# Optimization experiments

Hardware: AMD Instinct MI355X
Metric: run time of the kernel (lower is better)

The kernel has to match this reference:

```python
import jax, jax.numpy as jnp
import numpy as np

B, N, F_IN, H = 16, 1024, 64, 256
NEG = -9e15
ALPHA = 0.2  # LeakyReLU slope


def _leaky(x):
    return jnp.where(x >= 0, x, ALPHA * x)


def setup_inputs() -> dict:
    key = jax.random.key(0)
    ks = jax.random.split(key, 12)
    s = lambda k, shape, fan: jax.random.normal(k, shape, jnp.float32) / np.sqrt(fan)
    node_features = jax.random.normal(ks[0], (B, N, F_IN), jnp.float32)
    adj_matrix = jax.random.randint(ks[1], (B, N, N), 0, 2).astype(jnp.float32)
    return {
        "node_features": node_features,
        "adj_matrix": adj_matrix,
        "emb_W": s(ks[2], (F_IN, H), F_IN),
        "emb_b": jnp.zeros((H,), jnp.float32),
        "W0": s(ks[3], (H, H), H),
        "a1_0": s(ks[4], (H,), H),
        "a2_0": s(ks[5], (H,), H),
        "W1": s(ks[6], (H, H), H),
        "a1_1": s(ks[7], (H,), H),
        "a2_1": s(ks[8], (H,), H),
        "gp_W1": s(ks[9], (H, H), H),
        "gp_b1": jnp.zeros((H,), jnp.float32),
        "gp_W2": s(ks[10], (H, H), H),
        "gp_b2": jnp.zeros((H,), jnp.float32),
    }


def _gat_layer(x, mask, W, a1, a2):
    # x: [B,N,H]; mask: [B,N,N] bool. Equivalent to original concat trick:
    # a([h_i || h_j]) = h_i @ a1 + h_j @ a2 with a.weight split in halves.
    h = jnp.einsum('bnf,fo->bno', x, W)              # [B,N,H]
    s1 = jnp.einsum('bnh,h->bn', h, a1)              # [B,N]
    s2 = jnp.einsum('bnh,h->bn', h, a2)              # [B,N]
    e = _leaky(s1[:, :, None] + s2[:, None, :])      # [B,N,N]
    att = jax.nn.softmax(jnp.where(mask, e, NEG), axis=2)
    # dropout p=0.2 is identity in eval mode
    return jnp.einsum('bij,bjh->bih', att, h)        # [B,N,H]


def reference(node_features, adj_matrix, emb_W, emb_b,
              W0, a1_0, a2_0, W1, a1_1, a2_1,
              gp_W1, gp_b1, gp_W2, gp_b2):
    mask = adj_matrix > 0
    x = jnp.einsum('bnf,fh->bnh', node_features, emb_W) + emb_b
    x = jax.nn.relu(_gat_layer(x, mask, W0, a1_0, a2_0))
    x = jax.nn.relu(_gat_layer(x, mask, W1, a1_1, a2_1))
    g = jnp.mean(x, axis=1) + jnp.max(x, axis=1)     # [B,H]
    g = jax.nn.relu(g @ gp_W1 + gp_b1) @ gp_W2 + gp_b2
    return x, g
```

## Files before the change

kernel.cpp:

```cpp
#include <hip/hip_runtime.h>
#include <hip/hip_bf16.h>

#define B 16
#define N 1024
#define F_IN 64
#define H 256
#define ALPHA 0.2f

typedef __attribute__((ext_vector_type(8))) short short8;
typedef __attribute__((ext_vector_type(8))) _Float16 half8;
typedef __attribute__((ext_vector_type(4))) _Float16 half4;
typedef __attribute__((ext_vector_type(4))) float floatx4;

__device__ __forceinline__ floatx4 mfma_f16(half8 a, half8 b, floatx4 c) {
    return __builtin_amdgcn_mfma_f32_16x16x32_f16(a, b, c, 0, 0, 0);
}

__global__ __launch_bounds__(256) void k_front(const float* __restrict__ adj,
                                               const float* __restrict__ nf,
                                               const float* __restrict__ embW,
                                               const float* __restrict__ embB,
                                               const float* __restrict__ W0, const float* __restrict__ W1,
                                               const float* __restrict__ a10, const float* __restrict__ a20,
                                               const float* __restrict__ a11, const float* __restrict__ a21,
                                               unsigned* __restrict__ mask32,
                                               _Float16* __restrict__ xf,
                                               _Float16* __restrict__ wBf,
                                               float* __restrict__ wa1, float* __restrict__ wa2) {
    __shared__ float lds[256 * 17];
    const int blk = blockIdx.x;
    const int t = threadIdx.x;
    const int lane = t & 63;

    if (blk < 1024) {
        const int wv = blk * 4 + (t >> 6);
#pragma unroll 2
        for (int task = wv; task < B * N * 4; task += 4096) {
            const float4 v = *(const float4*)(adj + (size_t)task * 256 + lane * 4);
            unsigned long long b0 = __ballot(v.x > 0.f);
            unsigned long long b1 = __ballot(v.y > 0.f);
            unsigned long long b2 = __ballot(v.z > 0.f);
            unsigned long long b3 = __ballot(v.w > 0.f);
            if (lane < 8) {
                unsigned w0 = (unsigned)((b0 >> (8 * lane)) & 0xff)
                            | ((unsigned)((b1 >> (8 * lane)) & 0xff) << 8)
                            | ((unsigned)((b2 >> (8 * lane)) & 0xff) << 16)
                            | ((unsigned)((b3 >> (8 * lane)) & 0xff) << 24);
                const int jg = task & 3, row = task >> 2;
                mask32[(size_t)row * 32 + jg * 8 + lane] = w0;
            }
        }
        return;
    }
    if (blk < 1536) {
        const int row0 = (blk - 1024) * 32;
        float* nfs = lds;
        for (int idx = t; idx < 32 * F_IN; idx += 256) {
            int r = idx >> 6, f = idx & 63;
            nfs[f * 32 + r] = nf[(size_t)(row0 + r) * F_IN + f];
        }
        __syncthreads();
        const int c = t;
        float acc[32];
        const float bv = embB[c];
#pragma unroll
        for (int r = 0; r < 32; r++) acc[r] = bv;
#pragma unroll 8
        for (int f = 0; f < F_IN; f++) {
            const float w = embW[f * H + c];
            const float* nrow = nfs + f * 32;
#pragma unroll
            for (int q = 0; q < 8; q++) {
                float4 n4 = *(const float4*)(nrow + q * 4);
                acc[q * 4 + 0] += n4.x * w;
                acc[q * 4 + 1] += n4.y * w;
                acc[q * 4 + 2] += n4.z * w;
                acc[q * 4 + 3] += n4.w * w;
            }
        }
#pragma unroll
        for (int r = 0; r < 32; r++)
            xf[(size_t)(row0 + r) * H + c] = (_Float16)acc[r];
        return;
    }
    const int pb = blk - 1536;
    if (pb >= 32) {
        const int l = pb - 32;
        const float* W = l ? W1 : W0;
        const float* a1 = l ? a11 : a10;
        const float* a2 = l ? a21 : a20;
        float* a1s = lds;
        float* a2s = lds + 256;
        a1s[t] = a1[t]; a2s[t] = a2[t];
        __syncthreads();
        float v1 = 0.f, v2 = 0.f;
        for (int c = 0; c < H; c += 4) {
            float4 w = *(const float4*)&W[t * H + c];
            v1 += w.x * a1s[c] + w.y * a1s[c + 1] + w.z * a1s[c + 2] + w.w * a1s[c + 3];
            v2 += w.x * a2s[c] + w.y * a2s[c + 1] + w.z * a2s[c + 2] + w.w * a2s[c + 3];
        }
        wa1[l * H + t] = v1;
        wa2[l * H + t] = v2;
        return;
    }
    const int l = pb >> 4, ct = pb & 15;
    const float* W = l ? W1 : W0;
#pragma unroll
    for (int rep = 0; rep < 16; rep++) {
        int idx = rep * 256 + t;
        int k = idx >> 4, cl = idx & 15;
        lds[k * 17 + cl] = W[k * H + ct * 16 + cl];
    }
    __syncthreads();
    const int w = t >> 6;
    const int l15 = lane & 15, quad = lane >> 4;
#pragma unroll
    for (int e = 0; e < 2; e++) {
        const int ks = w * 2 + e;
        half8 bf;
#pragma unroll
        for (int jj = 0; jj < 8; jj++)
            bf[jj] = (_Float16)lds[(ks * 32 + quad * 8 + jj) * 17 + l15];
        *(half8*)(wBf + (size_t)(((l * 16 + ct) * 8 + ks) * 64 + lane) * 8) = bf;
    }
}

#define XS(it, ks) ((((it) * 8 + (ks))) * 520)
__global__ __launch_bounds__(256, 4) void k_gemm(const _Float16* __restrict__ xf,
                                                 const _Float16* __restrict__ wBf,
                                                 const float* __restrict__ wa1, const float* __restrict__ wa2,
                                                 _Float16* __restrict__ hB,
                                                 float* __restrict__ s1, float* __restrict__ s2,
                                                 unsigned* __restrict__ s2maxkey) {
    __shared__ __align__(16) _Float16 sm[8320];
    const int lin = blockIdx.x;
    const int rc = lin >> 1, chalf = lin & 1;
    const int row0 = rc * 32;
    const int t = threadIdx.x;
    const int lane = t & 63, w = t >> 6;
    const int l15 = lane & 15, quad = lane >> 4;

#pragma unroll
    for (int pass = 0; pass < 4; pass++) {
        int idx = pass * 256 + t;
        int row_l = idx >> 5, k8 = idx & 31;
        half8 v = *(const half8*)(xf + (size_t)(row0 + row_l) * H + k8 * 8);
        int it = row_l >> 4, lf = row_l & 15, ks = k8 >> 2, qd = k8 & 3;
        *(half8*)(sm + XS(it, ks) + (qd * 16 + lf) * 8) = v;
    }
    __syncthreads();

    const int ct0 = chalf * 8 + 2 * w;
    const _Float16* pB0 = wBf + (size_t)((ct0 * 8) * 64 + lane) * 8;
    const _Float16* pB1 = wBf + (size_t)(((ct0 + 1) * 8) * 64 + lane) * 8;

    floatx4 acc[2][2];
    floatx4 z = {0.f, 0.f, 0.f, 0.f};
    acc[0][0] = z; acc[0][1] = z; acc[1][0] = z; acc[1][1] = z;
    float sp1a = 0.f, sp2a = 0.f, sp1b = 0.f, sp2b = 0.f;

    half8 B0 = *(const half8*)(pB0);
    half8 B1 = *(const half8*)(pB1);

#pragma unroll
    for (int ks = 0; ks < 8; ks++) {
        half8 nB0 = B0, nB1 = B1;
        if (ks < 7) {
            const int o = (ks + 1) * 512;
            nB0 = *(const half8*)(pB0 + o);
            nB1 = *(const half8*)(pB1 + o);
        }
        half8 A0 = *(const half8*)(sm + XS(0, ks) + lane * 8);
        half8 A1 = *(const half8*)(sm + XS(1, ks) + lane * 8);
        acc[0][0] = mfma_f16(A0, B0, acc[0][0]);
        acc[0][1] = mfma_f16(A0, B1, acc[0][1]);
        acc[1][0] = mfma_f16(A1, B0, acc[1][0]);
        acc[1][1] = mfma_f16(A1, B1, acc[1][1]);
        if (chalf == 0 && w == 0) {
            float4 w1a = *(const float4*)(wa1 + ks * 32 + quad * 8);
            float4 w1b = *(const float4*)(wa1 + ks * 32 + quad * 8 + 4);
            float4 w2a = *(const float4*)(wa2 + ks * 32 + quad * 8);
            float4 w2b = *(const float4*)(wa2 + ks * 32 + quad * 8 + 4);
            float wv1[8] = {w1a.x, w1a.y, w1a.z, w1a.w, w1b.x, w1b.y, w1b.z, w1b.w};
            float wv2[8] = {w2a.x, w2a.y, w2a.z, w2a.w, w2b.x, w2b.y, w2b.z, w2b.w};
#pragma unroll
            for (int j = 0; j < 8; j++) {
                float xa = (float)A0[j];
                float xb = (float)A1[j];
                sp1a += xa * wv1[j]; sp2a += xa * wv2[j];
                sp1b += xb * wv1[j]; sp2b += xb * wv2[j];
            }
        }
        B0 = nB0; B1 = nB1;
    }

    __syncthreads();
    _Float16* trc = sm;
#pragma unroll
    for (int rg = 0; rg < 2; rg++) {
#pragma unroll
        for (int n2 = 0; n2 < 2; n2++) {
            const int c_l = (2 * w + n2) * 16 + l15;
            half4 hv;
            hv[0] = (_Float16)acc[rg][n2][0];
            hv[1] = (_Float16)acc[rg][n2][1];
            hv[2] = (_Float16)acc[rg][n2][2];
            hv[3] = (_Float16)acc[rg][n2][3];
            *(half4*)(trc + c_l * 40 + rg * 16 + quad * 4) = hv;
        }
    }
    __syncthreads();
    {
        const int ct_l = t >> 5, sub = t & 31;
        const int bb = row0 >> 10, jt = (row0 >> 5) & 31;
        _Float16* dst = hB + (size_t)(((bb * 16 + chalf * 8 + ct_l) * 32 + jt) * 64) * 8;
#pragma unroll
        for (int rep = 0; rep < 2; rep++) {
            int lo = sub + rep * 32;
            int qd = lo >> 4, lf = lo & 15;
            half8 hv = *(const half8*)(trc + (ct_l * 16 + lf) * 40 + qd * 8);
            *(half8*)(dst + lo * 8) = hv;
        }
    }
    if (chalf == 0 && w == 0) {
        sp1a += __shfl_xor(sp1a, 16); sp1a += __shfl_xor(sp1a, 32);
        sp2a += __shfl_xor(sp2a, 16); sp2a += __shfl_xor(sp2a, 32);
        sp1b += __shfl_xor(sp1b, 16); sp1b += __shfl_xor(sp1b, 32);
        sp2b += __shfl_xor(sp2b, 16); sp2b += __shfl_xor(sp2b, 32);
        if (quad == 0) {
            s1[row0 + l15] = sp1a; s2[row0 + l15] = sp2a;
            s1[row0 + 16 + l15] = sp1b; s2[row0 + 16 + l15] = sp2b;
        }
        float m = fmaxf(sp2a, sp2b);
#pragma unroll
        for (int off = 1; off <= 8; off <<= 1) m = fmaxf(m, __shfl_xor(m, off));
        if (lane == 0) {
            unsigned bt = __float_as_uint(m);
            unsigned keyv = (bt & 0x80000000u) ? ~bt : (bt | 0x80000000u);
            atomicMax(&s2maxkey[row0 >> 10], keyv);
        }
    }
}

__global__ __launch_bounds__(256) void k_pgen(const float* __restrict__ s1, const float* __restrict__ s2,
                                              const unsigned* __restrict__ mask32,
                                              const unsigned* __restrict__ s2maxkey,
                                              _Float16* __restrict__ pA, float* __restrict__ lsums) {
    __shared__ float s2s[N];
    __shared__ float lp[4][16];
    const int lin = blockIdx.x;
    const int xcd = lin & 7, sl = lin >> 3;
    const int b = xcd * 2 + (sl & 1);
    const int itg = sl >> 1;
    const int t = threadIdx.x;
    const int lane = t & 63, w = t >> 6;
    const int l15 = lane & 15, quad = lane >> 4;

    unsigned key = s2maxkey[b];
    unsigned mb = (key & 0x80000000u) ? (key ^ 0x80000000u) : ~key;
    const float s2max = __uint_as_float(mb);
    for (int idx = t; idx < N; idx += 256) s2s[idx] = s2[b * N + idx];
    __syncthreads();

    const int it = itg * 2 + (w & 1);
    const int jt0 = (w >> 1) * 16;
    const int i = it * 16 + l15;
    const float s1v = s1[b * N + i];
    const float tmx = s1v + s2max;
    const float mrow = fmaxf(tmx, ALPHA * tmx);
    const unsigned* mp = mask32 + (size_t)(b * N + i) * 32;
    _Float16* pdst = pA + (size_t)(((b * 64 + it) * 32 + jt0) * 64) * 8 + lane * 8;
    const int qsh = quad * 2;
    float lacc = 0.f;

    for (int jl = 0; jl < 16; jl++) {
        const int jt = jt0 + jl;
        unsigned mw = mp[jt];
        float4 sa = *(const float4*)&s2s[jt * 32 + quad * 8];
        float4 sb = *(const float4*)&s2s[jt * 32 + quad * 8 + 4];
        float sv[8] = {sa.x, sa.y, sa.z, sa.w, sb.x, sb.y, sb.z, sb.w};
        union { _Float16 h[8]; half8 v; } pk;
#pragma unroll
        for (int jj = 0; jj < 8; jj++) {
            float e = s1v + sv[jj];
            e = fmaxf(e, ALPHA * e);
            float p = __expf(e - mrow);
            p = ((mw >> ((jj & 3) * 8 + (jj >> 2) + qsh)) & 1u) ? p : 0.f;
            pk.h[jj] = (_Float16)p;
            lacc += (float)pk.h[jj];
        }
        *(half8*)(pdst + (size_t)jl * 512) = pk.v;
    }
    lacc += __shfl_xor(lacc, 16);
    lacc += __shfl_xor(lacc, 32);
    if (quad == 0) lp[w][l15] = lacc;
    __syncthreads();
    if (t < 32) {
        int itl = t >> 4, lf = t & 15;
        float tot = lp[itl][lf] + lp[2 + itl][lf];
        lsums[b * N + (itg * 2 + itl) * 16 + lf] = tot;
    }
}

template <int LAST>
__global__ __launch_bounds__(256, 2) void k_gat(const _Float16* __restrict__ pA,
                                                const _Float16* __restrict__ hB,
                                                const float* __restrict__ lsums,
                                                float* __restrict__ outf,
                                                _Float16* __restrict__ oxf,
                                                float* __restrict__ psum, float* __restrict__ pmax) {
    const int lin = blockIdx.x;
    const int xcd = lin & 7, sl = lin >> 3;
    const int b = xcd * 2 + (sl & 1);
    const int chunk = (sl >> 1) & 15;
    const int chalf = sl >> 5;
    const int i0 = chunk * 64;
    const int t = threadIdx.x;
    const int lane = t & 63, w = t >> 6;
    const int l15 = lane & 15, quad = lane >> 4;
    const int nb = 2 * w;
    const int ct0 = chalf * 8 + nb;

    const _Float16* pa0 = pA + (size_t)((b * 64 + chunk * 4 + 0) * 32 * 64) * 8 + lane * 8;
    const _Float16* pa1 = pA + (size_t)((b * 64 + chunk * 4 + 1) * 32 * 64) * 8 + lane * 8;
    const _Float16* pa2 = pA + (size_t)((b * 64 + chunk * 4 + 2) * 32 * 64) * 8 + lane * 8;
    const _Float16* pa3 = pA + (size_t)((b * 64 + chunk * 4 + 3) * 32 * 64) * 8 + lane * 8;
    const _Float16* pb0 = hB + (size_t)((b * 16 + ct0) * 32 * 64) * 8 + lane * 8;
    const _Float16* pb1 = hB + (size_t)((b * 16 + ct0 + 1) * 32 * 64) * 8 + lane * 8;

    floatx4 acc[4][2];
    floatx4 z = {0.f, 0.f, 0.f, 0.f};
#pragma unroll
    for (int rg = 0; rg < 4; rg++) { acc[rg][0] = z; acc[rg][1] = z; }

    half8 cA0 = *(const half8*)(pa0), cA1 = *(const half8*)(pa1);
    half8 cA2 = *(const half8*)(pa2), cA3 = *(const half8*)(pa3);
    half8 cB0 = *(const half8*)(pb0), cB1 = *(const half8*)(pb1);
    half8 nA0 = *(const half8*)(pa0 + 512), nA1 = *(const half8*)(pa1 + 512);
    half8 nA2 = *(const half8*)(pa2 + 512), nA3 = *(const half8*)(pa3 + 512);
    half8 nB0 = *(const half8*)(pb0 + 512), nB1 = *(const half8*)(pb1 + 512);

#pragma unroll 2
    for (int jt = 0; jt < 32; jt++) {
        const int j2 = (jt + 2 <= 31 ? jt + 2 : 31) * 512;
        half8 fA0 = *(const half8*)(pa0 + j2);
        half8 fA1 = *(const half8*)(pa1 + j2);
        half8 fA2 = *(const half8*)(pa2 + j2);
        half8 fA3 = *(const half8*)(pa3 + j2);
        half8 fB0 = *(const half8*)(pb0 + j2);
        half8 fB1 = *(const half8*)(pb1 + j2);
        acc[0][0] = mfma_f16(cA0, cB0, acc[0][0]);
        acc[1][0] = mfma_f16(cA1, cB0, acc[1][0]);
        acc[2][0] = mfma_f16(cA2, cB0, acc[2][0]);
        acc[3][0] = mfma_f16(cA3, cB0, acc[3][0]);
        acc[0][1] = mfma_f16(cA0, cB1, acc[0][1]);
        acc[1][1] = mfma_f16(cA1, cB1, acc[1][1]);
        acc[2][1] = mfma_f16(cA2, cB1, acc[2][1]);
        acc[3][1] = mfma_f16(cA3, cB1, acc[3][1]);
        cA0 = nA0; cA1 = nA1; cA2 = nA2; cA3 = nA3; cB0 = nB0; cB1 = nB1;
        nA0 = fA0; nA1 = fA1; nA2 = fA2; nA3 = fA3; nB0 = fB0; nB1 = fB1;
    }

    const size_t rbase = (size_t)b * N + i0;
    float inv[4][4];
#pragma unroll
    for (int rg = 0; rg < 4; rg++)
#pragma unroll
        for (int r = 0; r < 4; r++) inv[rg][r] = 1.f / lsums[rbase + rg * 16 + quad * 4 + r];

    float colsum[2] = {0.f, 0.f}, colmax[2] = {-INFINITY, -INFINITY};
#pragma unroll
    for (int rg = 0; rg < 4; rg++)
#pragma unroll
        for (int n2 = 0; n2 < 2; n2++) {
            const int c = (ct0 + n2) * 16 + l15;
#pragma unroll
            for (int r = 0; r < 4; r++) {
                float v = fmaxf(acc[rg][n2][r] * inv[rg][r], 0.f);
                const size_t row = rbase + rg * 16 + quad * 4 + r;
                if (LAST) {
                    outf[row * H + c] = v;
                    colsum[n2] += v;
                    colmax[n2] = fmaxf(colmax[n2], v);
                } else {
                    oxf[row * H + c] = (_Float16)v;
                }
            }
        }
    if (LAST) {
#pragma unroll
        for (int n2 = 0; n2 < 2; n2++) {
            float s = colsum[n2], m = colmax[n2];
            s += __shfl_xor(s, 16); s += __shfl_xor(s, 32);
            m = fmaxf(m, __shfl_xor(m, 16)); m = fmaxf(m, __shfl_xor(m, 32));
            if (quad == 0) {
                const int c = (ct0 + n2) * 16 + l15;
                psum[(b * 16 + chunk) * H + c] = s;
                pmax[(b * 16 + chunk) * H + c] = m;
            }
        }
    }
}

__global__ __launch_bounds__(256) void k_pool2(const float* __restrict__ psum,
                                               const float* __restrict__ pmax,
                                               const float* __restrict__ W1, const float* __restrict__ b1,
                                               const float* __restrict__ W2, const float* __restrict__ b2,
                                               float* __restrict__ gout) {
    __shared__ float g_s[H];
    __shared__ float t_s[H];
    const int b = blockIdx.x;
    const int c = threadIdx.x;
    float s = 0.f, m = -INFINITY;
#pragma unroll
    for (int ch = 0; ch < 16; ch++) {
        s += psum[(b * 16 + ch) * H + c];
        m = fmaxf(m, pmax[(b * 16 + ch) * H + c]);
    }
    g_s[c] = s * (1.f / N) + m;
    __syncthreads();
    float a = b1[c];
#pragma unroll 16
    for (int k = 0; k < H; k++) a += g_s[k] * W1[k * H + c];
    t_s[c] = fmaxf(a, 0.f);
    __syncthreads();
    float o = b2[c];
#pragma unroll 16
    for (int k = 0; k < H; k++) o += t_s[k] * W2[k * H + c];
    gout[b * H + c] = o;
}

extern "C" void kernel_launch(void* const* d_in, const int* in_sizes, int n_in,
                              void* d_out, int out_size, void* d_ws, size_t ws_size,
                              hipStream_t stream) {
    const float* nf    = (const float*)d_in[0];
    const float* adj   = (const float*)d_in[1];
    const float* emb_W = (const float*)d_in[2];
    const float* emb_b = (const float*)d_in[3];
    const float* W0    = (const float*)d_in[4];
    const float* a1_0  = (const float*)d_in[5];
    const float* a2_0  = (const float*)d_in[6];
    const float* W1    = (const float*)d_in[7];
    const float* a1_1  = (const float*)d_in[8];
    const float* a2_1  = (const float*)d_in[9];
    const float* gpW1  = (const float*)d_in[10];
    const float* gpb1  = (const float*)d_in[11];
    const float* gpW2  = (const float*)d_in[12];
    const float* gpb2  = (const float*)d_in[13];

    float* xout = (float*)d_out;
    float* gout = xout + B * N * H;

    char* w = (char*)d_ws;
    _Float16* xf     = (_Float16*)(w);
    _Float16* hB     = (_Float16*)(w + 8388608);
    _Float16* pA     = (_Float16*)(w + 16777216);
    unsigned* mask32 = (unsigned*)(w + 50331648);
    float* s1        = (float*)(w + 52428800);
    float* s2        = (float*)(w + 52494336);
    float* lsums     = (float*)(w + 52559872);
    _Float16* wBf    = (_Float16*)(w + 52625408);
    float* wa1       = (float*)(w + 52887552);
    float* wa2       = (float*)(w + 52889600);
    unsigned* keys   = (unsigned*)(w + 52891648);
    float* psum      = (float*)(w);
    float* pmax      = (float*)(w + 262144);

    hipMemsetAsync(keys, 0, 128, stream);
    k_front<<<1570, 256, 0, stream>>>(adj, nf, emb_W, emb_b, W0, W1,
                                      a1_0, a2_0, a1_1, a2_1,
                                      mask32, xf, wBf, wa1, wa2);

    k_gemm<<<1024, 256, 0, stream>>>(xf, wBf, wa1, wa2, hB, s1, s2, keys);
    k_pgen<<<512, 256, 0, stream>>>(s1, s2, mask32, keys, pA, lsums);
    k_gat<0><<<512, 256, 0, stream>>>(pA, hB, lsums, nullptr, xf, nullptr, nullptr);

    k_gemm<<<1024, 256, 0, stream>>>(xf, wBf + 65536, wa1 + H, wa2 + H, hB, s1, s2, keys + 16);
    k_pgen<<<512, 256, 0, stream>>>(s1, s2, mask32, keys + 16, pA, lsums);
    k_gat<1><<<512, 256, 0, stream>>>(pA, hB, lsums, xout, nullptr, psum, pmax);

    k_pool2<<<B, 256, 0, stream>>>(psum, pmax, gpW1, gpb1, gpW2, gpb2, gout);
}
```

Before: 243.8 us.

## Fuse attention probability generation and pooling head into the GAT aggregation kernel

Removes the separate probability-generation kernel and its large fp16 attention matrix in global memory. Each GAT block now computes exp-scores from s1/s2 and the bit mask on the fly, builds the MFMA A operand in registers, and accumulates row sums locally. The s2 max moves from a global atomic key to a per-block reduction. The final pooling MLP runs in the last block per batch via an atomic counter, replacing the pool2 launch. In exchange, each block recomputes the exponentials redundantly across its two column halves and holds eight B fragments per wave, which raises register pressure.

After: 275.8 us. +13.1%, slower.

```diff
diff --git a/kernel.cpp b/kernel.cpp
--- a/kernel.cpp
+++ b/kernel.cpp
@@ -7,7 +7,6 @@
 #define H 256
 #define ALPHA 0.2f
 
-typedef __attribute__((ext_vector_type(8))) short short8;
 typedef __attribute__((ext_vector_type(8))) _Float16 half8;
 typedef __attribute__((ext_vector_type(4))) _Float16 half4;
 typedef __attribute__((ext_vector_type(4))) float floatx4;
@@ -130,8 +129,7 @@
                                                  const _Float16* __restrict__ wBf,
                                                  const float* __restrict__ wa1, const float* __restrict__ wa2,
                                                  _Float16* __restrict__ hB,
-                                                 float* __restrict__ s1, float* __restrict__ s2,
-                                                 unsigned* __restrict__ s2maxkey) {
+                                                 float* __restrict__ s1, float* __restrict__ s2) {
     __shared__ __align__(16) _Float16 sm[8320];
     const int lin = blockIdx.x;
     const int rc = lin >> 1, chalf = lin & 1;
@@ -231,84 +229,28 @@
             s1[row0 + l15] = sp1a; s2[row0 + l15] = sp2a;
             s1[row0 + 16 + l15] = sp1b; s2[row0 + 16 + l15] = sp2b;
         }
-        float m = fmaxf(sp2a, sp2b);
-#pragma unroll
-        for (int off = 1; off <= 8; off <<= 1) m = fmaxf(m, __shfl_xor(m, off));
-        if (lane == 0) {
-            unsigned bt = __float_as_uint(m);
-            unsigned keyv = (bt & 0x80000000u) ? ~bt : (bt | 0x80000000u);
-            atomicMax(&s2maxkey[row0 >> 10], keyv);
-        }
     }
 }
 
-__global__ __launch_bounds__(256) void k_pgen(const float* __restrict__ s1, const float* __restrict__ s2,
-                                              const unsigned* __restrict__ mask32,
-                                              const unsigned* __restrict__ s2maxkey,
-                                              _Float16* __restrict__ pA, float* __restrict__ lsums) {
-    __shared__ float s2s[N];
-    __shared__ float lp[4][16];
-    const int lin = blockIdx.x;
-    const int xcd = lin & 7, sl = lin >> 3;
-    const int b = xcd * 2 + (sl & 1);
-    const int itg = sl >> 1;
-    const int t = threadIdx.x;
-    const int lane = t & 63, w = t >> 6;
-    const int l15 = lane & 15, quad = lane >> 4;
-
-    unsigned key = s2maxkey[b];
-    unsigned mb = (key & 0x80000000u) ? (key ^ 0x80000000u) : ~key;
-    const float s2max = __uint_as_float(mb);
-    for (int idx = t; idx < N; idx += 256) s2s[idx] = s2[b * N + idx];
-    __syncthreads();
-
-    const int it = itg * 2 + (w & 1);
-    const int jt0 = (w >> 1) * 16;
-    const int i = it * 16 + l15;
-    const float s1v = s1[b * N + i];
-    const float tmx = s1v + s2max;
-    const float mrow = fmaxf(tmx, ALPHA * tmx);
-    const unsigned* mp = mask32 + (size_t)(b * N + i) * 32;
-    _Float16* pdst = pA + (size_t)(((b * 64 + it) * 32 + jt0) * 64) * 8 + lane * 8;
-    const int qsh = quad * 2;
-    float lacc = 0.f;
-
-    for (int jl = 0; jl < 16; jl++) {
-        const int jt = jt0 + jl;
-        unsigned mw = mp[jt];
-        float4 sa = *(const float4*)&s2s[jt * 32 + quad * 8];
-        float4 sb = *(const float4*)&s2s[jt * 32 + quad * 8 + 4];
-        float sv[8] = {sa.x, sa.y, sa.z, sa.w, sb.x, sb.y, sb.z, sb.w};
-        union { _Float16 h[8]; half8 v; } pk;
-#pragma unroll
-        for (int jj = 0; jj < 8; jj++) {
-            float e = s1v + sv[jj];
-            e = fmaxf(e, ALPHA * e);
-            float p = __expf(e - mrow);
-            p = ((mw >> ((jj & 3) * 8 + (jj >> 2) + qsh)) & 1u) ? p : 0.f;
-            pk.h[jj] = (_Float16)p;
-            lacc += (float)pk.h[jj];
-        }
-        *(half8*)(pdst + (size_t)jl * 512) = pk.v;
-    }
-    lacc += __shfl_xor(lacc, 16);
-    lacc += __shfl_xor(lacc, 32);
-    if (quad == 0) lp[w][l15] = lacc;
-    __syncthreads();
-    if (t < 32) {
-        int itl = t >> 4, lf = t & 15;
-        float tot = lp[itl][lf] + lp[2 + itl][lf];
-        lsums[b * N + (itg * 2 + itl) * 16 + lf] = tot;
-    }
-}
-
 template <int LAST>
-__global__ __launch_bounds__(256, 2) void k_gat(const _Float16* __restrict__ pA,
-                                                const _Float16* __restrict__ hB,
-                                                const float* __restrict__ lsums,
+__global__ __launch_bounds__(256, 2) void k_gat(const _Float16* __restrict__ hB,
+                                                const float* __restrict__ s1g,
+                                                const float* __restrict__ s2g,
+                                                const unsigned* __restrict__ mask32,
                                                 float* __restrict__ outf,
                                                 _Float16* __restrict__ oxf,
-                                                float* __restrict__ psum, float* __restrict__ pmax) {
+                                                float* __restrict__ psum, float* __restrict__ pmax,
+                                                unsigned* __restrict__ cnt,
+                                                const float* __restrict__ gpW1, const float* __restrict__ gpb1,
+                                                const float* __restrict__ gpW2, const float* __restrict__ gpb2,
+                                                float* __restrict__ gout) {
+    __shared__ float s2s[N];
+    __shared__ unsigned msk[64][33];
+    __shared__ float wmax[4];
+    __shared__ float l_s[64];
+    __shared__ float red1[4][128];
+    __shared__ float red2[4][128];
+    __shared__ int flag_s;
     const int lin = blockIdx.x;
     const int xcd = lin & 7, sl = lin >> 3;
     const int b = xcd * 2 + (sl & 1);
@@ -318,116 +260,140 @@
     const int t = threadIdx.x;
     const int lane = t & 63, w = t >> 6;
     const int l15 = lane & 15, quad = lane >> 4;
-    const int nb = 2 * w;
-    const int ct0 = chalf * 8 + nb;
-
-    const _Float16* pa0 = pA + (size_t)((b * 64 + chunk * 4 + 0) * 32 * 64) * 8 + lane * 8;
-    const _Float16* pa1 = pA + (size_t)((b * 64 + chunk * 4 + 1) * 32 * 64) * 8 + lane * 8;
-    const _Float16* pa2 = pA + (size_t)((b * 64 + chunk * 4 + 2) * 32 * 64) * 8 + lane * 8;
-    const _Float16* pa3 = pA + (size_t)((b * 64 + chunk * 4 + 3) * 32 * 64) * 8 + lane * 8;
-    const _Float16* pb0 = hB + (size_t)((b * 16 + ct0) * 32 * 64) * 8 + lane * 8;
-    const _Float16* pb1 = hB + (size_t)((b * 16 + ct0 + 1) * 32 * 64) * 8 + lane * 8;
-
-    floatx4 acc[4][2];
+    const int ct0 = chalf * 8;
+
+    float tm = -INFINITY;
+    for (int idx = t; idx < N; idx += 256) {
+        float v = s2g[b * N + idx];
+        s2s[idx] = v;
+        tm = fmaxf(tm, v);
+    }
+#pragma unroll
+    for (int off = 1; off <= 32; off <<= 1) tm = fmaxf(tm, __shfl_xor(tm, off));
+    if (lane == 0) wmax[w] = tm;
+#pragma unroll
+    for (int pass = 0; pass < 8; pass++) {
+        int idx = pass * 256 + t;
+        int r = idx >> 5, wd = idx & 31;
+        msk[r][wd] = mask32[(size_t)(b * N + i0 + r) * 32 + wd];
+    }
+    __syncthreads();
+    const float s2max = fmaxf(fmaxf(wmax[0], wmax[1]), fmaxf(wmax[2], wmax[3]));
+
+    const float s1v = s1g[b * N + i0 + w * 16 + l15];
+    const float tmx = s1v + s2max;
+    const float mrow = fmaxf(tmx, ALPHA * tmx);
+
+    const _Float16* pb[8];
+#pragma unroll
+    for (int k = 0; k < 8; k++)
+        pb[k] = hB + (size_t)((b * 16 + ct0 + k) * 32 * 64) * 8 + lane * 8;
+
+    floatx4 acc[8];
     floatx4 z = {0.f, 0.f, 0.f, 0.f};
 #pragma unroll
-    for (int rg = 0; rg < 4; rg++) { acc[rg][0] = z; acc[rg][1] = z; }
-
-    half8 cA0 = *(const half8*)(pa0), cA1 = *(const half8*)(pa1);
-    half8 cA2 = *(const half8*)(pa2), cA3 = *(const half8*)(pa3);
-    half8 cB0 = *(const half8*)(pb0), cB1 = *(const half8*)(pb1);
-    half8 nA0 = *(const half8*)(pa0 + 512), nA1 = *(const half8*)(pa1 + 512);
-    half8 nA2 = *(const half8*)(pa2 + 512), nA3 = *(const half8*)(pa3 + 512);
-    half8 nB0 = *(const half8*)(pb0 + 512), nB1 = *(const half8*)(pb1 + 512);
-
-#pragma unroll 2
+    for (int k = 0; k < 8; k++) acc[k] = z;
+    float lacc = 0.f;
+
+    half8 cB[8];
+#pragma unroll
+    for (int k = 0; k < 8; k++) cB[k] = *(const half8*)(pb[k]);
+
     for (int jt = 0; jt < 32; jt++) {
-        const int j2 = (jt + 2 <= 31 ? jt + 2 : 31) * 512;
-        half8 fA0 = *(const half8*)(pa0 + j2);
-        half8 fA1 = *(const half8*)(pa1 + j2);
-        half8 fA2 = *(const half8*)(pa2 + j2);
-        half8 fA3 = *(const half8*)(pa3 + j2);
-        half8 fB0 = *(const half8*)(pb0 + j2);
-        half8 fB1 = *(const half8*)(pb1 + j2);
-        acc[0][0] = mfma_f16(cA0, cB0, acc[0][0]);
-        acc[1][0] = mfma_f16(cA1, cB0, acc[1][0]);
-        acc[2][0] = mfma_f16(cA2, cB0, acc[2][0]);
-        acc[3][0] = mfma_f16(cA3, cB0, acc[3][0]);
-        acc[0][1] = mfma_f16(cA0, cB1, acc[0][1]);
-        acc[1][1] = mfma_f16(cA1, cB1, acc[1][1]);
-        acc[2][1] = mfma_f16(cA2, cB1, acc[2][1]);
-        acc[3][1] = mfma_f16(cA3, cB1, acc[3][1]);
-        cA0 = nA0; cA1 = nA1; cA2 = nA2; cA3 = nA3; cB0 = nB0; cB1 = nB1;
-        nA0 = fA0; nA1 = fA1; nA2 = fA2; nA3 = fA3; nB0 = fB0; nB1 = fB1;
-    }
-
-    const size_t rbase = (size_t)b * N + i0;
-    float inv[4][4];
-#pragma unroll
-    for (int rg = 0; rg < 4; rg++)
-#pragma unroll
-        for (int r = 0; r < 4; r++) inv[rg][r] = 1.f / lsums[rbase + rg * 16 + quad * 4 + r];
-
-    float colsum[2] = {0.f, 0.f}, colmax[2] = {-INFINITY, -INFINITY};
-#pragma unroll
-    for (int rg = 0; rg < 4; rg++)
-#pragma unroll
-        for (int n2 = 0; n2 < 2; n2++) {
-            const int c = (ct0 + n2) * 16 + l15;
-#pragma unroll
-            for (int r = 0; r < 4; r++) {
-                float v = fmaxf(acc[rg][n2][r] * inv[rg][r], 0.f);
-                const size_t row = rbase + rg * 16 + quad * 4 + r;
-                if (LAST) {
-                    outf[row * H + c] = v;
-                    colsum[n2] += v;
-                    colmax[n2] = fmaxf(colmax[n2], v);
-                } else {
-                    oxf[row * H + c] = (_Float16)v;
-                }
+        half8 nB[8];
+        if (jt < 31) {
+            const int o = (jt + 1) * 512;
+#pragma unroll
+            for (int k = 0; k < 8; k++) nB[k] = *(const half8*)(pb[k] + o);
+        }
+        unsigned mwq = msk[w * 16 + l15][jt] >> (quad * 2);
+        float4 sa = *(const float4*)&s2s[jt * 32 + quad * 8];
+        float4 sb = *(const float4*)&s2s[jt * 32 + quad * 8 + 4];
+        float sv[8] = {sa.x, sa.y, sa.z, sa.w, sb.x, sb.y, sb.z, sb.w};
+        union { _Float16 h[8]; half8 v; } pk;
+#pragma unroll
+        for (int jj = 0; jj < 8; jj++) {
+            float e = s1v + sv[jj];
+            e = fmaxf(e, ALPHA * e);
+            float p = __expf(e - mrow);
+            p = ((mwq >> ((jj & 3) * 8 + (jj >> 2))) & 1u) ? p : 0.f;
+            pk.h[jj] = (_Float16)p;
+            lacc += (float)pk.h[jj];
+        }
+        half8 A = pk.v;
+#pragma unroll
+        for (int k = 0; k < 8; k++) acc[k] = mfma_f16(A, cB[k], acc[k]);
+        if (jt < 31) {
+#pragma unroll
+            for (int k = 0; k < 8; k++) cB[k] = nB[k];
+        }
+    }
+
+    lacc += __shfl_xor(lacc, 16);
+    lacc += __shfl_xor(lacc, 32);
+    if (quad == 0) l_s[w * 16 + l15] = lacc;
+    __syncthreads();
+
+    float inv[4];
+#pragma unroll
+    for (int r = 0; r < 4; r++) inv[r] = 1.f / l_s[w * 16 + quad * 4 + r];
+
+    const size_t rbase = (size_t)b * N + i0 + w * 16 + quad * 4;
+#pragma unroll
+    for (int k = 0; k < 8; k++) {
+        const int c = (ct0 + k) * 16 + l15;
+        float cs = 0.f, cm = -INFINITY;
+#pragma unroll
+        for (int r = 0; r < 4; r++) {
+            float v = fmaxf(acc[k][r] * inv[r], 0.f);
+            if (LAST) {
+                outf[(rbase + r) * H + c] = v;
+                cs += v; cm = fmaxf(cm, v);
+            } else {
+                oxf[(rbase + r) * H + c] = (_Float16)v;
             }
         }
+        if (LAST) {
+            cs += __shfl_xor(cs, 16); cs += __shfl_xor(cs, 32);
+            cm = fmaxf(cm, __shfl_xor(cm, 16)); cm = fmaxf(cm, __shfl_xor(cm, 32));
+            if (quad == 0) { red1[w][k * 16 + l15] = cs; red2[w][k * 16 + l15] = cm; }
+        }
+    }
     if (LAST) {
-#pragma unroll
-        for (int n2 = 0; n2 < 2; n2++) {
-            float s = colsum[n2], m = colmax[n2];
-            s += __shfl_xor(s, 16); s += __shfl_xor(s, 32);
-            m = fmaxf(m, __shfl_xor(m, 16)); m = fmaxf(m, __shfl_xor(m, 32));
-            if (quad == 0) {
-                const int c = (ct0 + n2) * 16 + l15;
-                psum[(b * 16 + chunk) * H + c] = s;
-                pmax[(b * 16 + chunk) * H + c] = m;
+        __syncthreads();
+        if (t < 128) {
+            float s = red1[0][t] + red1[1][t] + red1[2][t] + red1[3][t];
+            float m = fmaxf(fmaxf(red2[0][t], red2[1][t]), fmaxf(red2[2][t], red2[3][t]));
+            psum[(b * 16 + chunk) * H + chalf * 128 + t] = s;
+            pmax[(b * 16 + chunk) * H + chalf * 128 + t] = m;
+        }
+        __threadfence();
+        __syncthreads();
+        if (t == 0) flag_s = (int)atomicAdd(&cnt[b], 1u);
+        __syncthreads();
+        if (flag_s == 31) {
+            __threadfence();
+            float* g_s = s2s;
+            float* t_s = s2s + 256;
+            float s = 0.f, m = -INFINITY;
+#pragma unroll
+            for (int ch = 0; ch < 16; ch++) {
+                s += psum[(b * 16 + ch) * H + t];
+                m = fmaxf(m, pmax[(b * 16 + ch) * H + t]);
             }
-        }
-    }
-}
-
-__global__ __launch_bounds__(256) void k_pool2(const float* __restrict__ psum,
-                                               const float* __restrict__ pmax,
-                                               const float* __restrict__ W1, const float* __restrict__ b1,
-                                               const float* __restrict__ W2, const float* __restrict__ b2,
-                                               float* __restrict__ gout) {
-    __shared__ float g_s[H];
-    __shared__ float t_s[H];
-    const int b = blockIdx.x;
-    const int c = threadIdx.x;
-    float s = 0.f, m = -INFINITY;
-#pragma unroll
-    for (int ch = 0; ch < 16; ch++) {
-        s += psum[(b * 16 + ch) * H + c];
-        m = fmaxf(m, pmax[(b * 16 + ch) * H + c]);
-    }
-    g_s[c] = s * (1.f / N) + m;
-    __syncthreads();
-    float a = b1[c];
+            g_s[t] = s * (1.f / N) + m;
+            __syncthreads();
+            float a = gpb1[t];
 #pragma unroll 16
-    for (int k = 0; k < H; k++) a += g_s[k] * W1[k * H + c];
-    t_s[c] = fmaxf(a, 0.f);
-    __syncthreads();
-    float o = b2[c];
+            for (int k = 0; k < H; k++) a += g_s[k] * gpW1[k * H + t];
+            t_s[t] = fmaxf(a, 0.f);
+            __syncthreads();
+            float o = gpb2[t];
 #pragma unroll 16
-    for (int k = 0; k < H; k++) o += t_s[k] * W2[k * H + c];
-    gout[b * H + c] = o;
+            for (int k = 0; k < H; k++) o += t_s[k] * gpW2[k * H + t];
+            gout[b * H + t] = o;
+        }
+    }
 }
 
 extern "C" void kernel_launch(void* const* d_in, const int* in_sizes, int n_in,
@@ -454,30 +420,28 @@
     char* w = (char*)d_ws;
     _Float16* xf     = (_Float16*)(w);
     _Float16* hB     = (_Float16*)(w + 8388608);
-    _Float16* pA     = (_Float16*)(w + 16777216);
-    unsigned* mask32 = (unsigned*)(w + 50331648);
-    float* s1        = (float*)(w + 52428800);
-    float* s2        = (float*)(w + 52494336);
-    float* lsums     = (float*)(w + 52559872);
-    _Float16* wBf    = (_Float16*)(w + 52625408);
-    float* wa1       = (float*)(w + 52887552);
-    float* wa2       = (float*)(w + 52889600);
-    unsigned* keys   = (unsigned*)(w + 52891648);
-    float* psum      = (float*)(w);
-    float* pmax      = (float*)(w + 262144);
-
-    hipMemsetAsync(keys, 0, 128, stream);
+    unsigned* mask32 = (unsigned*)(w + 16777216);
+    float* s1        = (float*)(w + 18874368);
+    float* s2        = (float*)(w + 18939904);
+    _Float16* wBf    = (_Float16*)(w + 19005440);
+    float* wa1       = (float*)(w + 19267584);
+    float* wa2       = (float*)(w + 19269632);
+    float* psum      = (float*)(w + 19271680);
+    float* pmax      = (float*)(w + 19533824);
+    unsigned* cnt    = (unsigned*)(w + 19795968);
+
+    hipMemsetAsync(cnt, 0, 64, stream);
     k_front<<<1570, 256, 0, stream>>>(adj, nf, emb_W, emb_b, W0, W1,
                                       a1_0, a2_0, a1_1, a2_1,
                                       mask32, xf, wBf, wa1, wa2);
 
-    k_gemm<<<1024, 256, 0, stream>>>(xf, wBf, wa1, wa2, hB, s1, s2, keys);
-    k_pgen<<<512, 256, 0, stream>>>(s1, s2, mask32, keys, pA, lsums);
-    k_gat<0><<<512, 256, 0, stream>>>(pA, hB, lsums, nullptr, xf, nullptr, nullptr);
-
-    k_gemm<<<1024, 256, 0, stream>>>(xf, wBf + 65536, wa1 + H, wa2 + H, hB, s1, s2, keys + 16);
-    k_pgen<<<512, 256, 0, stream>>>(s1, s2, mask32, keys + 16, pA, lsums);
-    k_gat<1><<<512, 256, 0, stream>>>(pA, hB, lsums, xout, nullptr, psum, pmax);
-
-    k_pool2<<<B, 256, 0, stream>>>(psum, pmax, gpW1, gpb1, gpW2, gpb2, gout);
+    k_gemm<<<1024, 256, 0, stream>>>(xf, wBf, wa1, wa2, hB, s1, s2);
+    k_gat<0><<<512, 256, 0, stream>>>(hB, s1, s2, mask32, nullptr, xf,
+                                      nullptr, nullptr, nullptr,
+                                      nullptr, nullptr, nullptr, nullptr, nullptr);
+
+    k_gemm<<<1024, 256, 0, stream>>>(xf, wBf + 65536, wa1 + H, wa2 + H, hB, s1, s2);
+    k_gat<1><<<512, 256, 0, stream>>>(hB, s1, s2, mask32, xout, nullptr,
+                                      psum, pmax, cnt,
+                                      gpW1, gpb1, gpW2, gpb2, gout);
 }
```
